# Kernel tuning notes

Measured on AMD Instinct MI355X. Metric: run time of the kernel, lower is better.

## Reference

```python
import jax, jax.numpy as jnp
import numpy as np

BN_EPS = 1e-5
NEG_SLOPE = 0.2


def _add_self_loops(edge_index, n):
    loops = jnp.arange(n, dtype=edge_index.dtype)
    src = jnp.concatenate([edge_index[0], loops])
    dst = jnp.concatenate([edge_index[1], loops])
    return src, dst


def _batchnorm(h, g, b):
    mean = h.mean(axis=0)
    var = h.var(axis=0)  # biased, as in BN forward
    return (h - mean) * jax.lax.rsqrt(var + BN_EPS) * g + b


def _gat_conv(x, edge_index, W, att_src, att_dst, bias):
    # heads=2, concat=False (mean over heads), add_self_loops=True
    n = x.shape[0]
    H, F = att_src.shape
    xp = (x @ W).reshape(n, H, F)                      # [N,H,F]
    a_src = jnp.einsum('nhf,hf->nh', xp, att_src)      # [N,H]
    a_dst = jnp.einsum('nhf,hf->nh', xp, att_dst)
    src, dst = _add_self_loops(edge_index, n)
    e = jax.nn.leaky_relu(a_src[src] + a_dst[dst], NEG_SLOPE)  # [Et,H]
    emax = jax.ops.segment_max(e, dst, num_segments=n)[dst]
    ex = jnp.exp(e - emax)
    denom = jax.ops.segment_sum(ex, dst, num_segments=n)[dst]
    alpha = ex / denom                                 # softmax per dst node
    msg = xp[src] * alpha[..., None]                   # [Et,H,F]
    out = jax.ops.segment_sum(msg, dst, num_segments=n)
    return out.mean(axis=1) + bias                     # [N,F]


def _gcn_conv(x, edge_index, W, bias):
    n = x.shape[0]
    xp = x @ W
    src, dst = _add_self_loops(edge_index, n)
    deg = jax.ops.segment_sum(jnp.ones_like(src, dtype=xp.dtype), dst, num_segments=n)
    dinv = jnp.where(deg > 0, jax.lax.rsqrt(jnp.maximum(deg, 1.0)), 0.0)
    norm = dinv[src] * dinv[dst]                       # [Et]
    out = jax.ops.segment_sum(xp[src] * norm[:, None], dst, num_segments=n)
    return out + bias


def setup_inputs() -> dict:
    key = jax.random.key(0)
    ks = jax.random.split(key, 16)
    N, E, D_IN, HID, LAT, DEC = 50000, 800000, 256, 128, 64, 256
    s = lambda fan: 1.0 / np.sqrt(fan)
    inp = {
        'x': jax.random.normal(ks[0], (N, D_IN), jnp.float32),
        'edge_index': jax.random.randint(ks[1], (2, E), 0, N, dtype=jnp.int32),
        'gat_W': jax.random.normal(ks[2], (D_IN, 2 * HID), jnp.float32) * s(D_IN),
        'gat_att_src': jax.random.normal(ks[3], (2, HID), jnp.float32) * s(HID),
        'gat_att_dst': jax.random.normal(ks[4], (2, HID), jnp.float32) * s(HID),
        'gat_bias': jnp.zeros((HID,), jnp.float32),
        'bn1_g': jnp.ones((HID,), jnp.float32),
        'bn1_b': jnp.zeros((HID,), jnp.float32),
        'gcn_W': jax.random.normal(ks[5], (HID, LAT), jnp.float32) * s(HID),
        'gcn_bias': jnp.zeros((LAT,), jnp.float32),
        'bn2_g': jnp.ones((LAT,), jnp.float32),
        'bn2_b': jnp.zeros((LAT,), jnp.float32),
        'mu_W': jax.random.normal(ks[6], (LAT, LAT), jnp.float32) * s(LAT),
        'mu_b': jnp.zeros((LAT,), jnp.float32),
        'lv_W': jax.random.normal(ks[7], (LAT, LAT), jnp.float32) * s(LAT),
        'lv_b': jnp.zeros((LAT,), jnp.float32),
        'res_W': jax.random.normal(ks[8], (LAT, LAT), jnp.float32) * s(LAT),
        'res_b': jnp.zeros((LAT,), jnp.float32),
        'dec_W1': jax.random.normal(ks[9], (2 * LAT, DEC), jnp.float32) * s(2 * LAT),
        'dec_b1': jnp.zeros((DEC,), jnp.float32),
        'dec_W2': jax.random.normal(ks[10], (DEC, 1), jnp.float32) * s(DEC),
        'dec_b2': jnp.zeros((1,), jnp.float32),
        'eps': jax.random.normal(ks[11], (N, LAT), jnp.float32),
    }
    return inp


def reference(x, edge_index, gat_W, gat_att_src, gat_att_dst, gat_bias,
              bn1_g, bn1_b, gcn_W, gcn_bias, bn2_g, bn2_b,
              mu_W, mu_b, lv_W, lv_b, res_W, res_b,
              dec_W1, dec_b1, dec_W2, dec_b2, eps):
    # encode (dropout omitted: eval mode; BN uses batch statistics)
    h = jax.nn.relu(_gat_conv(x, edge_index, gat_W, gat_att_src, gat_att_dst, gat_bias))
    h = _batchnorm(h, bn1_g, bn1_b)
    h = jax.nn.relu(_gcn_conv(h, edge_index, gcn_W, gcn_bias))
    h = _batchnorm(h, bn2_g, bn2_b)
    mu = h @ mu_W + mu_b
    logvar = h @ lv_W + lv_b
    # reparameterize
    z = mu + eps * jnp.exp(0.5 * logvar)
    # decode: edge-gather -> residual linear -> concat -> MLP
    res_z = z @ res_W + res_b
    row, col = edge_index[0], edge_index[1]
    e_emb = jnp.concatenate([res_z[row], res_z[col]], axis=1)  # [E, 2*LAT]
    hdec = jax.nn.relu(e_emb @ dec_W1 + dec_b1)
    recon = (hdec @ dec_W2 + dec_b2)[:, 0]
    return recon, mu, logvar
```

## Files before the change

### kernel.cpp

```cpp
#include <hip/hip_runtime.h>
#include <math.h>

constexpr int DIN = 256;
constexpr int HID = 128;
constexpr int LAT = 64;

typedef short bfrag __attribute__((ext_vector_type(8)));
typedef float f32x4 __attribute__((ext_vector_type(4)));

__device__ __forceinline__ float4 ld4(const float* p) { return *reinterpret_cast<const float4*>(p); }
__device__ __forceinline__ void st4(float* p, float4 v) { *reinterpret_cast<float4*>(p) = v; }

__device__ __forceinline__ unsigned short f2bf(float f) {
  unsigned int u = __float_as_uint(f);
  unsigned int r = (u + 0x7FFFu + ((u >> 16) & 1u)) >> 16;
  return (unsigned short)r;
}

__device__ __forceinline__ float bf2f(unsigned short u) {
  return __uint_as_float(((unsigned int)u) << 16);
}

__global__ __launch_bounds__(256) void gemm64b(const float* __restrict__ A, const float* __restrict__ B,
                                               const float* __restrict__ crow, unsigned short* __restrict__ Cb,
                                               int M, int N, int K) {
  __shared__ float As[32][68];
  __shared__ float Bs[32][68];
  int t = threadIdx.x;
  int m0 = blockIdx.x * 64, n0 = blockIdx.y * 64;
  int tm = t & 15, tn = t >> 4;
  float acc[4][4];
#pragma unroll
  for (int i = 0; i < 4; i++)
#pragma unroll
    for (int j = 0; j < 4; j++) acc[i][j] = 0.f;

  for (int kt = 0; kt < K; kt += 32) {
#pragma unroll
    for (int i = 0; i < 2; ++i) {
      int f4 = t + i * 256;
      int m = f4 >> 3;
      int k4 = (f4 & 7) << 2;
      int gm = m0 + m;
      float4 v = make_float4(0.f, 0.f, 0.f, 0.f);
      if (gm < M) v = ld4(A + (size_t)gm * K + kt + k4);
      As[k4 + 0][m] = v.x; As[k4 + 1][m] = v.y; As[k4 + 2][m] = v.z; As[k4 + 3][m] = v.w;
    }
#pragma unroll
    for (int i = 0; i < 2; ++i) {
      int f4 = t + i * 256;
      int k = f4 >> 4;
      int n4 = (f4 & 15) << 2;
      float4 v = ld4(B + (size_t)(kt + k) * N + n0 + n4);
      st4(&Bs[k][n4], v);
    }
    __syncthreads();
#pragma unroll
    for (int k = 0; k < 32; ++k) {
      float4 a = ld4(&As[k][tm << 2]);
      float4 b = ld4(&Bs[k][tn << 2]);
      float av[4] = {a.x, a.y, a.z, a.w};
      float bv[4] = {b.x, b.y, b.z, b.w};
#pragma unroll
      for (int i = 0; i < 4; i++)
#pragma unroll
        for (int j = 0; j < 4; j++) acc[i][j] = fmaf(av[i], bv[j], acc[i][j]);
    }
    __syncthreads();
  }
#pragma unroll
  for (int i = 0; i < 4; ++i) {
    int gm = m0 + (tm << 2) + i;
    if (gm < M) {
      int nb = n0 + (tn << 2);
      ushort4 o;
      o.x = f2bf(acc[i][0] + crow[nb]);
      o.y = f2bf(acc[i][1] + crow[nb + 1]);
      o.z = f2bf(acc[i][2] + crow[nb + 2]);
      o.w = f2bf(acc[i][3] + crow[nb + 3]);
      *(ushort4*)(Cb + (size_t)gm * N + nb) = o;
    }
  }
}

__global__ __launch_bounds__(256) void gemm_xp_mfma(const float* __restrict__ xf,
                                                    const unsigned short* __restrict__ Wtb,
                                                    const float* __restrict__ att_src,
                                                    const float* __restrict__ att_dst,
                                                    unsigned short* __restrict__ xpb,
                                                    float* __restrict__ a_src, float* __restrict__ a_dst, int M) {
  __shared__ unsigned short Als[64 * 256];
  __shared__ unsigned short Bls[64 * 256];
  int t = threadIdx.x;
  int wv = t >> 6, l = t & 63, lg = l >> 4, ll = l & 15;
  int cg = blockIdx.x;
  int rt = blockIdx.y;

  {
    int row = t >> 2, seg = t & 3;
    int gr = min(rt * 64 + row, M - 1);
    const float4* src = (const float4*)(xf + (size_t)gr * 256 + seg * 64);
    int swz = (row & 7) << 4;
#pragma unroll
    for (int c = 0; c < 8; ++c) {
      float4 a = src[2 * c], b = src[2 * c + 1];
      uint4 v;
      v.x = (unsigned)f2bf(a.x) | ((unsigned)f2bf(a.y) << 16);
      v.y = (unsigned)f2bf(a.z) | ((unsigned)f2bf(a.w) << 16);
      v.z = (unsigned)f2bf(b.x) | ((unsigned)f2bf(b.y) << 16);
      v.w = (unsigned)f2bf(b.z) | ((unsigned)f2bf(b.w) << 16);
      int bo = seg * 128 + c * 16;
      *(uint4*)((char*)Als + row * 512 + (bo ^ swz)) = v;
    }
  }
  {
    int col = t >> 2, seg = t & 3;
    const uint4* src = (const uint4*)(Wtb + (size_t)(cg * 64 + col) * 256 + seg * 64);
    int swz = (col & 7) << 4;
#pragma unroll
    for (int c = 0; c < 8; ++c) {
      int bo = seg * 128 + c * 16;
      *(uint4*)((char*)Bls + col * 512 + (bo ^ swz)) = src[c];
    }
  }
  __syncthreads();

  f32x4 acc[4];
#pragma unroll
  for (int i = 0; i < 4; ++i) acc[i] = (f32x4){0.f, 0.f, 0.f, 0.f};

#pragma unroll
  for (int kt = 0; kt < 8; ++kt) {
    int ar = wv * 16 + ll;
    bfrag af = *(const bfrag*)((char*)Als + ar * 512 + ((kt * 64 + lg * 16) ^ ((ar & 7) << 4)));
#pragma unroll
    for (int fn = 0; fn < 4; ++fn) {
      int bc = fn * 16 + ll;
      bfrag bf = *(const bfrag*)((char*)Bls + bc * 512 + ((kt * 64 + lg * 16) ^ ((bc & 7) << 4)));
      acc[fn] = __builtin_amdgcn_mfma_f32_16x16x32_bf16(af, bf, acc[fn], 0, 0, 0);
    }
  }

#pragma unroll
  for (int fn = 0; fn < 4; ++fn) {
#pragma unroll
    for (int r = 0; r < 4; ++r) {
      int row = rt * 64 + wv * 16 + lg * 4 + r;
      if (row < M) xpb[(size_t)row * 512 + cg * 64 + fn * 16 + ll] = f2bf(acc[fn][r]);
    }
  }

  int h = cg >> 1;
  int c0 = (cg & 1) * 64;
  float asv[4], adv[4];
#pragma unroll
  for (int fn = 0; fn < 4; ++fn) {
    asv[fn] = att_src[h * 128 + c0 + fn * 16 + ll];
    adv[fn] = att_dst[h * 128 + c0 + fn * 16 + ll];
  }
  float ps[4] = {0.f, 0.f, 0.f, 0.f}, pd[4] = {0.f, 0.f, 0.f, 0.f};
#pragma unroll
  for (int fn = 0; fn < 4; ++fn)
#pragma unroll
    for (int r = 0; r < 4; ++r) {
      ps[r] = fmaf(acc[fn][r], asv[fn], ps[r]);
      pd[r] = fmaf(acc[fn][r], adv[fn], pd[r]);
    }
#pragma unroll
  for (int m = 8; m >= 1; m >>= 1) {
#pragma unroll
    for (int r = 0; r < 4; ++r) { ps[r] += __shfl_xor(ps[r], m); pd[r] += __shfl_xor(pd[r], m); }
  }
  if (ll == 0) {
#pragma unroll
    for (int r = 0; r < 4; ++r) {
      int row = rt * 64 + wv * 16 + lg * 4 + r;
      if (row < M) {
        atomicAdd(&a_src[row * 2 + h], ps[r]);
        atomicAdd(&a_dst[row * 2 + h], pd[r]);
      }
    }
  }
}

__global__ void deg_count(const int* __restrict__ ei, int E, int Et, int* __restrict__ deg) {
  int i = blockIdx.x * blockDim.x + threadIdx.x;
  if (i >= Et) return;
  int d = (i < E) ? ei[E + i] : (i - E);
  atomicAdd(&deg[d], 1);
}

__global__ __launch_bounds__(256) void bsum_kernel(const int* __restrict__ deg, int N, int* __restrict__ bsum) {
  int t = threadIdx.x;
  int i = blockIdx.x * 256 + t;
  int v = (i < N) ? deg[i] : 0;
#pragma unroll
  for (int m = 32; m >= 1; m >>= 1) v += __shfl_xor(v, m);
  __shared__ int sh[4];
  if ((t & 63) == 0) sh[t >> 6] = v;
  __syncthreads();
  if (t == 0) bsum[blockIdx.x] = sh[0] + sh[1] + sh[2] + sh[3];
}

__global__ __launch_bounds__(256) void bscan_kernel(int* __restrict__ bsum, int B) {
  __shared__ int sh[256];
  int t = threadIdx.x;
  int v = (t < B) ? bsum[t] : 0;
  sh[t] = v;
  __syncthreads();
  for (int d = 1; d < 256; d <<= 1) {
    int x = (t >= d) ? sh[t - d] : 0;
    __syncthreads();
    sh[t] += x;
    __syncthreads();
  }
  if (t < B) bsum[t] = sh[t] - v;
}

__global__ __launch_bounds__(256) void scan_apply(const int* __restrict__ deg, const int* __restrict__ bsum, int N,
                                                  int* __restrict__ offs, int* __restrict__ cursor,
                                                  float* __restrict__ dinv) {
  int t = threadIdx.x;
  int i = blockIdx.x * 256 + t;
  int v = (i < N) ? deg[i] : 0;
  __shared__ int sh[256];
  sh[t] = v;
  __syncthreads();
  for (int d = 1; d < 256; d <<= 1) {
    int x = (t >= d) ? sh[t - d] : 0;
    __syncthreads();
    sh[t] += x;
    __syncthreads();
  }
  if (i < N) {
    int off = bsum[blockIdx.x] + sh[t] - v;
    offs[i] = off;
    cursor[i] = off;
    dinv[i] = rsqrtf((float)v);
  }
}

__global__ void csr_fill(const int* __restrict__ ei, int E, int Et, int* __restrict__ cursor, int* __restrict__ csr) {
  int i = blockIdx.x * blockDim.x + threadIdx.x;
  if (i >= Et) return;
  int s, d;
  if (i < E) { s = ei[i]; d = ei[E + i]; } else { s = i - E; d = i - E; }
  int pos = atomicAdd(&cursor[d], 1);
  csr[pos] = s;
}

__global__ __launch_bounds__(256) void gat_fused(const int* __restrict__ offs, const int* __restrict__ deg,
                                                 const int* __restrict__ csr, const float* __restrict__ a_src,
                                                 const float* __restrict__ a_dst,
                                                 const unsigned short* __restrict__ xpb,
                                                 const float* __restrict__ bias,
                                                 float* __restrict__ h1, int N) {
  int wid = threadIdx.x >> 6, lane = threadIdx.x & 63;
  int n = blockIdx.x * 4 + wid;
  if (n >= N) return;
  int off = offs[n], dg = deg[n];
  float ad0 = a_dst[n * 2], ad1 = a_dst[n * 2 + 1];
  const float2* as2 = (const float2*)a_src;

  float4 acc = make_float4(0.f, 0.f, 0.f, 0.f);
  float s0 = 0.f, s1 = 0.f;
  bool h0 = lane < 32;

#define GAT_STEP(aa, uu)                                         \
  {                                                              \
    float e0 = (aa).x + ad0; e0 = e0 >= 0.f ? e0 : 0.2f * e0;    \
    float e1 = (aa).y + ad1; e1 = e1 >= 0.f ? e1 : 0.2f * e1;    \
    float x0 = __expf(e0), x1 = __expf(e1);                      \
    s0 += x0; s1 += x1;                                          \
    float xa = h0 ? x0 : x1;                                     \
    acc.x = fmaf(bf2f((uu).x), xa, acc.x);                       \
    acc.y = fmaf(bf2f((uu).y), xa, acc.y);                       \
    acc.z = fmaf(bf2f((uu).z), xa, acc.z);                       \
    acc.w = fmaf(bf2f((uu).w), xa, acc.w);                       \
  }

  int k = 0;
  for (; k + 8 <= dg; k += 8) {
    int s_[8];
#pragma unroll
    for (int q = 0; q < 8; ++q) s_[q] = csr[off + k + q];
    float2 a_[8];
    ushort4 u_[8];
#pragma unroll
    for (int q = 0; q < 8; ++q) a_[q] = as2[s_[q]];
#pragma unroll
    for (int q = 0; q < 8; ++q) u_[q] = ((const ushort4*)(xpb + (size_t)s_[q] * 512))[lane];
#pragma unroll
    for (int q = 0; q < 8; ++q) GAT_STEP(a_[q], u_[q]);
  }
  for (; k + 4 <= dg; k += 4) {
    int sa = csr[off + k], sb = csr[off + k + 1], sc = csr[off + k + 2], sd = csr[off + k + 3];
    float2 aa = as2[sa], ab = as2[sb], ac = as2[sc], ad = as2[sd];
    ushort4 ua = ((const ushort4*)(xpb + (size_t)sa * 512))[lane];
    ushort4 ub = ((const ushort4*)(xpb + (size_t)sb * 512))[lane];
    ushort4 uc = ((const ushort4*)(xpb + (size_t)sc * 512))[lane];
    ushort4 ud = ((const ushort4*)(xpb + (size_t)sd * 512))[lane];
    GAT_STEP(aa, ua); GAT_STEP(ab, ub); GAT_STEP(ac, uc); GAT_STEP(ad, ud);
  }
  for (; k < dg; ++k) {
    int s = csr[off + k];
    float2 a = as2[s];
    ushort4 u = ((const ushort4*)(xpb + (size_t)s * 512))[lane];
    GAT_STEP(a, u);
  }
#undef GAT_STEP

  float r = h0 ? (1.f / s0) : (1.f / s1);
  acc.x *= r; acc.y *= r; acc.z *= r; acc.w *= r;

  float ox = __shfl_down(acc.x, 32);
  float oy = __shfl_down(acc.y, 32);
  float oz = __shfl_down(acc.z, 32);
  float ow = __shfl_down(acc.w, 32);
  if (h0) {
    int f4 = lane << 2;
    float4 b = ld4(bias + f4);
    float4 o;
    o.x = fmaxf(0.f, (acc.x + ox) * 0.5f + b.x);
    o.y = fmaxf(0.f, (acc.y + oy) * 0.5f + b.y);
    o.z = fmaxf(0.f, (acc.z + oz) * 0.5f + b.z);
    o.w = fmaxf(0.f, (acc.w + ow) * 0.5f + b.w);
    st4(h1 + (size_t)n * 128 + f4, o);
  }
}

template <int C>
__global__ __launch_bounds__(256) void bn_stats(const float* __restrict__ h, int N, float* __restrict__ P,
                                                float* __restrict__ PS) {
  constexpr int R = 256 / C;
  __shared__ float sh[256], sh2[256];
  int t = threadIdx.x;
  int c = t % C, r = t / C;
  float s = 0.f, ss = 0.f;
  for (int n = blockIdx.x * R + r; n < N; n += gridDim.x * R) {
    float v = h[(size_t)n * C + c];
    s += v; ss += v * v;
  }
  sh[t] = s; sh2[t] = ss;
  __syncthreads();
  if (r == 0) {
#pragma unroll
    for (int i = 1; i < R; ++i) { s += sh[i * C + c]; ss += sh2[i * C + c]; }
    P[blockIdx.x * C + c] = s;
    PS[blockIdx.x * C + c] = ss;
  }
}

__global__ __launch_bounds__(256) void bn_fold_gcn(const float* __restrict__ P, const float* __restrict__ PS,
                                                   int G, int N, const float* __restrict__ g,
                                                   const float* __restrict__ b, const float* __restrict__ W,
                                                   float* __restrict__ Wf, float* __restrict__ cvec) {
  __shared__ float ssv[128], stv[128];
  int t = threadIdx.x;
  if (t < 128) {
    float s = 0.f, ss = 0.f;
    for (int i = 0; i < G; ++i) { s += P[i * 128 + t]; ss += PS[i * 128 + t]; }
    float mean = s / N;
    float var = ss / N - mean * mean;
    float sc = g[t] * rsqrtf(var + 1e-5f);
    ssv[t] = sc;
    stv[t] = b[t] - mean * sc;
  }
  __syncthreads();
  for (int i = t; i < 128 * 64; i += 256) {
    int k = i >> 6;
    Wf[i] = ssv[k] * W[i];
  }
  if (t < 64) {
    float c = 0.f;
    for (int k = 0; k < 128; ++k) c += stv[k] * W[k * 64 + t];
    cvec[t] = c;
  }
}

__global__ __launch_bounds__(256) void bn_fold_mulv(const float* __restrict__ P, const float* __restrict__ PS,
                                                    int G, int N, const float* __restrict__ g,
                                                    const float* __restrict__ b,
                                                    const float* __restrict__ Wmu, const float* __restrict__ mub,
                                                    const float* __restrict__ Wlv, const float* __restrict__ lvb,
                                                    float* __restrict__ Wmuf, float* __restrict__ cmu,
                                                    float* __restrict__ Wlvf, float* __restrict__ clv) {
  __shared__ float ssv[64], stv[64];
  int t = threadIdx.x;
  if (t < 64) {
    float s = 0.f, ss = 0.f;
    for (int i = 0; i < G; ++i) { s += P[i * 64 + t]; ss += PS[i * 64 + t]; }
    float mean = s / N;
    float var = ss / N - mean * mean;
    float sc = g[t] * rsqrtf(var + 1e-5f);
    ssv[t] = sc;
    stv[t] = b[t] - mean * sc;
  }
  __syncthreads();
  for (int i = t; i < 4096; i += 256) {
    int k = i >> 6;
    Wmuf[i] = ssv[k] * Wmu[i];
    Wlvf[i] = ssv[k] * Wlv[i];
  }
  if (t < 64) {
    float cm = mub[t], cl = lvb[t];
    for (int k = 0; k < 64; ++k) { cm += stv[k] * Wmu[k * 64 + t]; cl += stv[k] * Wlv[k * 64 + t]; }
    cmu[t] = cm; clv[t] = cl;
  }
}

__global__ __launch_bounds__(256) void gcn_aggregate_bf(const int* __restrict__ offs, const int* __restrict__ deg,
                                                        const int* __restrict__ csr,
                                                        const unsigned short* __restrict__ xpb2,
                                                        const float* __restrict__ dinv, const float* __restrict__ bias,
                                                        float* __restrict__ g2, int N) {
  int wid = threadIdx.x >> 6, lane = threadIdx.x & 63;
  int n = blockIdx.x * 4 + wid;
  if (n >= N) return;
  int off = offs[n], dg = deg[n];
  float acc = 0.f;
  int k = 0;
  for (; k + 8 <= dg; k += 8) {
    int s_[8];
#pragma unroll
    for (int q = 0; q < 8; ++q) s_[q] = csr[off + k + q];
    float d_[8];
    unsigned short u_[8];
#pragma unroll
    for (int q = 0; q < 8; ++q) d_[q] = dinv[s_[q]];
#pragma unroll
    for (int q = 0; q < 8; ++q) u_[q] = xpb2[(size_t)s_[q] * 64 + lane];
#pragma unroll
    for (int q = 0; q < 8; ++q) acc = fmaf(bf2f(u_[q]), d_[q], acc);
  }
  for (; k + 4 <= dg; k += 4) {
    int sa = csr[off + k], sb = csr[off + k + 1], sc = csr[off + k + 2], sd = csr[off + k + 3];
    float da = dinv[sa], db = dinv[sb], dc = dinv[sc], dd = dinv[sd];
    unsigned short ua = xpb2[(size_t)sa * 64 + lane];
    unsigned short ub = xpb2[(size_t)sb * 64 + lane];
    unsigned short uc = xpb2[(size_t)sc * 64 + lane];
    unsigned short ud = xpb2[(size_t)sd * 64 + lane];
    acc = fmaf(bf2f(ua), da, acc);
    acc = fmaf(bf2f(ub), db, acc);
    acc = fmaf(bf2f(uc), dc, acc);
    acc = fmaf(bf2f(ud), dd, acc);
  }
  for (; k < dg; ++k) {
    int s = csr[off + k];
    acc = fmaf(bf2f(xpb2[(size_t)s * 64 + lane]), dinv[s], acc);
  }
  float v = acc * dinv[n] + bias[lane];
  g2[(size_t)n * 64 + lane] = fmaxf(v, 0.f);
}

__global__ __launch_bounds__(256) void tail_fused(const float* __restrict__ g2,
                                                  const float* __restrict__ Wmuf, const float* __restrict__ cmu,
                                                  const float* __restrict__ Wlvf, const float* __restrict__ clv,
                                                  const float* __restrict__ resW, const float* __restrict__ resb,
                                                  const float* __restrict__ eps,
                                                  float* __restrict__ mu, float* __restrict__ lv,
                                                  unsigned short* __restrict__ rzb, int N) {
  __shared__ float Gs[64][68];
  __shared__ float Wm[64][64];
  __shared__ float Wl[64][64];
  __shared__ float Rw[64][64];
  int t = threadIdx.x;
  int m0 = blockIdx.x * 64;
  int tm = t & 15, tn = t >> 4;

#pragma unroll
  for (int i = 0; i < 4; ++i) {
    int f4 = t + i * 256;
    int row = f4 >> 4;
    int k4 = (f4 & 15) << 2;
    int gr = m0 + row;
    float4 v = make_float4(0.f, 0.f, 0.f, 0.f);
    if (gr < N) v = ld4(g2 + (size_t)gr * 64 + k4);
    Gs[k4 + 0][row] = v.x; Gs[k4 + 1][row] = v.y; Gs[k4 + 2][row] = v.z; Gs[k4 + 3][row] = v.w;
    st4(&Wm[f4 >> 4][k4], ld4(Wmuf + f4 * 4));
    st4(&Wl[f4 >> 4][k4], ld4(Wlvf + f4 * 4));
    st4(&Rw[f4 >> 4][k4], ld4(resW + f4 * 4));
  }
  __syncthreads();

  float am[4][4], al[4][4];
#pragma unroll
  for (int i = 0; i < 4; ++i)
#pragma unroll
    for (int j = 0; j < 4; ++j) { am[i][j] = 0.f; al[i][j] = 0.f; }

#pragma unroll 8
  for (int k = 0; k < 64; ++k) {
    float4 a = ld4(&Gs[k][tm << 2]);
    float4 bm = ld4(&Wm[k][tn << 2]);
    float4 bl = ld4(&Wl[k][tn << 2]);
    float av[4] = {a.x, a.y, a.z, a.w};
    float bmv[4] = {bm.x, bm.y, bm.z, bm.w};
    float blv[4] = {bl.x, bl.y, bl.z, bl.w};
#pragma unroll
    for (int i = 0; i < 4; ++i)
#pragma unroll
      for (int j = 0; j < 4; ++j) {
        am[i][j] = fmaf(av[i], bmv[j], am[i][j]);
        al[i][j] = fmaf(av[i], blv[j], al[i][j]);
      }
  }

  int nb = tn << 2;
  float cm4[4] = {cmu[nb], cmu[nb + 1], cmu[nb + 2], cmu[nb + 3]};
  float cl4[4] = {clv[nb], clv[nb + 1], clv[nb + 2], clv[nb + 3]};
  float zreg[4][4];
#pragma unroll
  for (int i = 0; i < 4; ++i) {
    int gr = m0 + (tm << 2) + i;
    if (gr < N) {
      float4 ep = ld4(eps + (size_t)gr * 64 + nb);
      float epv[4] = {ep.x, ep.y, ep.z, ep.w};
      float muv[4], lvv[4];
#pragma unroll
      for (int j = 0; j < 4; ++j) {
        muv[j] = am[i][j] + cm4[j];
        lvv[j] = al[i][j] + cl4[j];
        zreg[i][j] = fmaf(epv[j], __expf(0.5f * lvv[j]), muv[j]);
      }
      st4(mu + (size_t)gr * 64 + nb, make_float4(muv[0], muv[1], muv[2], muv[3]));
      st4(lv + (size_t)gr * 64 + nb, make_float4(lvv[0], lvv[1], lvv[2], lvv[3]));
    } else {
#pragma unroll
      for (int j = 0; j < 4; ++j) zreg[i][j] = 0.f;
    }
  }

  __syncthreads();
#pragma unroll
  for (int i = 0; i < 4; ++i)
#pragma unroll
    for (int j = 0; j < 4; ++j) Gs[(tn << 2) + j][(tm << 2) + i] = zreg[i][j];
  __syncthreads();

  float ar[4][4];
#pragma unroll
  for (int i = 0; i < 4; ++i)
#pragma unroll
    for (int j = 0; j < 4; ++j) ar[i][j] = 0.f;
#pragma unroll 8
  for (int k = 0; k < 64; ++k) {
    float4 a = ld4(&Gs[k][tm << 2]);
    float4 b = ld4(&Rw[k][tn << 2]);
    float av[4] = {a.x, a.y, a.z, a.w};
    float bv[4] = {b.x, b.y, b.z, b.w};
#pragma unroll
    for (int i = 0; i < 4; ++i)
#pragma unroll
      for (int j = 0; j < 4; ++j) ar[i][j] = fmaf(av[i], bv[j], ar[i][j]);
  }
  float rb4[4] = {resb[nb], resb[nb + 1], resb[nb + 2], resb[nb + 3]};
#pragma unroll
  for (int i = 0; i < 4; ++i) {
    int gr = m0 + (tm << 2) + i;
    if (gr < N) {
      ushort4 o;
      o.x = f2bf(ar[i][0] + rb4[0]);
      o.y = f2bf(ar[i][1] + rb4[1]);
      o.z = f2bf(ar[i][2] + rb4[2]);
      o.w = f2bf(ar[i][3] + rb4[3]);
      *(ushort4*)(rzb + (size_t)gr * 64 + nb) = o;
    }
  }
}

__global__ void prep_gatW(const float* __restrict__ W, unsigned short* __restrict__ Wtb) {
  int i = blockIdx.x * blockDim.x + threadIdx.x;
  if (i >= 256 * 256) return;
  int col = i >> 8, k = i & 255;
  Wtb[i] = f2bf(W[k * 256 + col]);
}

__global__ void prep_W1(const float* __restrict__ W1, unsigned short* __restrict__ W1t) {
  int i = blockIdx.x * blockDim.x + threadIdx.x;
  if (i >= 4 * 256 * 40) return;
  int kt = i / 10240;
  int rem = i - kt * 10240;
  int j = rem / 40;
  int kp = rem - j * 40;
  float v = (kp < 32) ? W1[(size_t)(kt * 32 + kp) * 256 + j] : 0.f;
  W1t[i] = f2bf(v);
}

__global__ __launch_bounds__(256) void decoder_mfma(const int* __restrict__ ei, int E,
                                                    const unsigned short* __restrict__ rzb,
                                                    const unsigned short* __restrict__ W1t,
                                                    const float* __restrict__ b1, const float* __restrict__ W2,
                                                    const float* __restrict__ b2, float* __restrict__ recon) {
  __shared__ unsigned short Als[64 * 128];
  __shared__ unsigned short Bls[256 * 40];
  __shared__ float red[4][64];
  int t = threadIdx.x;
  int wv = t >> 6, l = t & 63;
  int lg = l >> 4, ll = l & 15;
  int e0 = blockIdx.x * 64;

  {
    int e = t >> 2;
    int part = (t >> 1) & 1;
    int half = t & 1;
    int eg = e0 + e;
    if (eg >= E) eg = E - 1;
    int r = (part == 0) ? ei[eg] : ei[E + eg];
    const uint4* gsrc = (const uint4*)(rzb + (size_t)r * 64 + half * 32);
    int bo0 = part * 128 + half * 64;
    int swz = (e & 7) << 4;
#pragma unroll
    for (int c = 0; c < 4; ++c) {
      uint4 v = gsrc[c];
      int bo = bo0 + c * 16;
      *(uint4*)&Als[e * 128 + ((bo ^ swz) >> 1)] = v;
    }
  }

  f32x4 acc[4][4];
#pragma unroll
  for (int a = 0; a < 4; ++a)
#pragma unroll
    for (int b = 0; b < 4; ++b) acc[a][b] = (f32x4){0.f, 0.f, 0.f, 0.f};

  for (int kt = 0; kt < 4; ++kt) {
    __syncthreads();
    {
      const uint4* gsrc = (const uint4*)(W1t + kt * 10240);
      uint4* ldst = (uint4*)Bls;
#pragma unroll
      for (int i = 0; i < 5; ++i) ldst[t + i * 256] = gsrc[t + i * 256];
    }
    __syncthreads();

    bfrag af[4];
#pragma unroll
    for (int fm = 0; fm < 4; ++fm) {
      int e = fm * 16 + ll;
      int bo = kt * 64 + lg * 16;
      af[fm] = *(const bfrag*)&Als[e * 128 + ((bo ^ ((e & 7) << 4)) >> 1)];
    }
#pragma unroll
    for (int fn = 0; fn < 4; ++fn) {
      int j = wv * 64 + fn * 16 + ll;
      bfrag bf = *(const bfrag*)&Bls[j * 40 + lg * 8];
#pragma unroll
      for (int fm = 0; fm < 4; ++fm)
        acc[fm][fn] = __builtin_amdgcn_mfma_f32_16x16x32_bf16(af[fm], bf, acc[fm][fn], 0, 0, 0);
    }
  }

  float bj[4], wj[4];
#pragma unroll
  for (int fn = 0; fn < 4; ++fn) {
    int j = wv * 64 + fn * 16 + ll;
    bj[fn] = b1[j];
    wj[fn] = W2[j];
  }
#pragma unroll
  for (int fm = 0; fm < 4; ++fm) {
    float pr[4] = {0.f, 0.f, 0.f, 0.f};
#pragma unroll
    for (int fn = 0; fn < 4; ++fn) {
#pragma unroll
      for (int r = 0; r < 4; ++r)
        pr[r] = fmaf(fmaxf(acc[fm][fn][r] + bj[fn], 0.f), wj[fn], pr[r]);
    }
#pragma unroll
    for (int m = 8; m >= 1; m >>= 1) {
#pragma unroll
      for (int r = 0; r < 4; ++r) pr[r] += __shfl_xor(pr[r], m);
    }
    if (ll == 0) {
#pragma unroll
      for (int r = 0; r < 4; ++r) red[wv][fm * 16 + lg * 4 + r] = pr[r];
    }
  }
  __syncthreads();
  if (t < 64) {
    int eg = e0 + t;
    if (eg < E) recon[eg] = red[0][t] + red[1][t] + red[2][t] + red[3][t] + b2[0];
  }
}

extern "C" void kernel_launch(void* const* d_in, const int* in_sizes, int n_in,
                              void* d_out, int out_size, void* d_ws, size_t ws_size,
                              hipStream_t stream) {
  const float* x = (const float*)d_in[0];
  const int* ei = (const int*)d_in[1];
  const float* gat_W = (const float*)d_in[2];
  const float* att_src = (const float*)d_in[3];
  const float* att_dst = (const float*)d_in[4];
  const float* gat_bias = (const float*)d_in[5];
  const float* bn1_g = (const float*)d_in[6];
  const float* bn1_b = (const float*)d_in[7];
  const float* gcn_W = (const float*)d_in[8];
  const float* gcn_bias = (const float*)d_in[9];
  const float* bn2_g = (const float*)d_in[10];
  const float* bn2_b = (const float*)d_in[11];
  const float* mu_W = (const float*)d_in[12];
  const float* mu_b = (const float*)d_in[13];
  const float* lv_W = (const float*)d_in[14];
  const float* lv_b = (const float*)d_in[15];
  const float* res_W = (const float*)d_in[16];
  const float* res_b = (const float*)d_in[17];
  const float* dec_W1 = (const float*)d_in[18];
  const float* dec_b1 = (const float*)d_in[19];
  const float* dec_W2 = (const float*)d_in[20];
  const float* dec_b2 = (const float*)d_in[21];
  const float* eps = (const float*)d_in[22];

  int N = in_sizes[0] / DIN;
  int E = in_sizes[1] / 2;
  int Et = E + N;
  int NB = (N + 255) / 256;

  float* ws = (float*)d_ws;
  size_t off = 0;
  float* xp = ws; off += (size_t)N * 256;
  unsigned short* xpb = (unsigned short*)xp;
  unsigned short* xpb2 = (unsigned short*)xp;
  float* g2 = xp + (size_t)N * 64;
  float* rz = xp + (size_t)N * 192;
  unsigned short* rzb = (unsigned short*)rz;
  float* h1 = ws + off; off += (size_t)N * 128;
  float* a_src = ws + off; off += (size_t)2 * N;
  float* a_dst = ws + off; off += (size_t)2 * N;
  float* dinv = ws + off; off += N;
  float* P = ws + off; off += 128 * 128;
  float* PS = ws + off; off += 128 * 128;
  float* W2f = ws + off; off += 128 * 64;
  float* c2 = ws + off; off += 64;
  float* Wmuf = ws + off; off += 64 * 64;
  float* cmu = ws + off; off += 64;
  float* Wlvf = ws + off; off += 64 * 64;
  float* clv = ws + off; off += 64;
  unsigned short* W1t = (unsigned short*)(ws + off); off += 20480;
  unsigned short* Wtb = (unsigned short*)(ws + off); off += 32768;
  int* deg = (int*)(ws + off); off += N;
  int* offs = (int*)(ws + off); off += N;
  int* cursor = (int*)(ws + off); off += N;
  int* bsum = (int*)(ws + off); off += 256;
  int* csr = (int*)(ws + off); off += Et;

  float* recon = (float*)d_out;
  float* mu = recon + E;
  float* lv = mu + (size_t)N * LAT;

  prep_W1<<<(4 * 256 * 40 + 255) / 256, 256, 0, stream>>>(dec_W1, W1t);
  prep_gatW<<<(256 * 256 + 255) / 256, 256, 0, stream>>>(gat_W, Wtb);
  hipMemsetAsync(a_src, 0, (size_t)4 * N * sizeof(float), stream);

  dim3 gX(4, (N + 63) / 64);
  gemm_xp_mfma<<<gX, 256, 0, stream>>>(x, Wtb, att_src, att_dst, xpb, a_src, a_dst, N);

  hipMemsetAsync(deg, 0, (size_t)N * sizeof(int), stream);
  deg_count<<<(Et + 255) / 256, 256, 0, stream>>>(ei, E, Et, deg);
  bsum_kernel<<<NB, 256, 0, stream>>>(deg, N, bsum);
  bscan_kernel<<<1, 256, 0, stream>>>(bsum, NB);
  scan_apply<<<NB, 256, 0, stream>>>(deg, bsum, N, offs, cursor, dinv);
  csr_fill<<<(Et + 255) / 256, 256, 0, stream>>>(ei, E, Et, cursor, csr);

  gat_fused<<<(N + 3) / 4, 256, 0, stream>>>(offs, deg, csr, a_src, a_dst, xpb, gat_bias, h1, N);

  bn_stats<128><<<128, 256, 0, stream>>>(h1, N, P, PS);
  bn_fold_gcn<<<1, 256, 0, stream>>>(P, PS, 128, N, bn1_g, bn1_b, gcn_W, W2f, c2);
  dim3 gB((N + 63) / 64, 1);
  gemm64b<<<gB, 256, 0, stream>>>(h1, W2f, c2, xpb2, N, 64, 128);

  gcn_aggregate_bf<<<(N + 3) / 4, 256, 0, stream>>>(offs, deg, csr, xpb2, dinv, gcn_bias, g2, N);

  bn_stats<64><<<128, 256, 0, stream>>>(g2, N, P, PS);
  bn_fold_mulv<<<1, 256, 0, stream>>>(P, PS, 128, N, bn2_g, bn2_b, mu_W, mu_b, lv_W, lv_b,
                                      Wmuf, cmu, Wlvf, clv);
  tail_fused<<<(N + 63) / 64, 256, 0, stream>>>(g2, Wmuf, cmu, Wlvf, clv, res_W, res_b, eps,
                                                mu, lv, rzb, N);

  decoder_mfma<<<(E + 63) / 64, 256, 0, stream>>>(ei, E, rzb, W1t, dec_b1, dec_W2, dec_b2, recon);
}
```

Before: 563.1 us.

## Use bf16 MFMA for GCN GEMM and split edge lists across half-waves

Replaces the scalar fp32 GEMM for the BN-folded GCN weight with a bf16 MFMA kernel. The folded weight is now stored transposed in bf16, and h1 is converted to bf16 in LDS. The GAT and GCN aggregation kernels now split each node's neighbor list between the two half-waves, each doing wider per-lane loads (uint4 / 32-bit), and combine partial sums and softmax denominators with shuffles. This aims to improve memory-level parallelism and cut per-edge instruction count. The cost is extra shuffles plus bf16 rounding of h1 and the weights inside the GEMM.

```diff
diff --git a/kernel.cpp b/kernel.cpp
--- a/kernel.cpp
+++ b/kernel.cpp
@@ -19,68 +19,6 @@
 
 __device__ __forceinline__ float bf2f(unsigned short u) {
   return __uint_as_float(((unsigned int)u) << 16);
-}
-
-__global__ __launch_bounds__(256) void gemm64b(const float* __restrict__ A, const float* __restrict__ B,
-                                               const float* __restrict__ crow, unsigned short* __restrict__ Cb,
-                                               int M, int N, int K) {
-  __shared__ float As[32][68];
-  __shared__ float Bs[32][68];
-  int t = threadIdx.x;
-  int m0 = blockIdx.x * 64, n0 = blockIdx.y * 64;
-  int tm = t & 15, tn = t >> 4;
-  float acc[4][4];
-#pragma unroll
-  for (int i = 0; i < 4; i++)
-#pragma unroll
-    for (int j = 0; j < 4; j++) acc[i][j] = 0.f;
-
-  for (int kt = 0; kt < K; kt += 32) {
-#pragma unroll
-    for (int i = 0; i < 2; ++i) {
-      int f4 = t + i * 256;
-      int m = f4 >> 3;
-      int k4 = (f4 & 7) << 2;
-      int gm = m0 + m;
-      float4 v = make_float4(0.f, 0.f, 0.f, 0.f);
-      if (gm < M) v = ld4(A + (size_t)gm * K + kt + k4);
-      As[k4 + 0][m] = v.x; As[k4 + 1][m] = v.y; As[k4 + 2][m] = v.z; As[k4 + 3][m] = v.w;
-    }
-#pragma unroll
-    for (int i = 0; i < 2; ++i) {
-      int f4 = t + i * 256;
-      int k = f4 >> 4;
-      int n4 = (f4 & 15) << 2;
-      float4 v = ld4(B + (size_t)(kt + k) * N + n0 + n4);
-      st4(&Bs[k][n4], v);
-    }
-    __syncthreads();
-#pragma unroll
-    for (int k = 0; k < 32; ++k) {
-      float4 a = ld4(&As[k][tm << 2]);
-      float4 b = ld4(&Bs[k][tn << 2]);
-      float av[4] = {a.x, a.y, a.z, a.w};
-      float bv[4] = {b.x, b.y, b.z, b.w};
-#pragma unroll
-      for (int i = 0; i < 4; i++)
-#pragma unroll
-        for (int j = 0; j < 4; j++) acc[i][j] = fmaf(av[i], bv[j], acc[i][j]);
-    }
-    __syncthreads();
-  }
-#pragma unroll
-  for (int i = 0; i < 4; ++i) {
-    int gm = m0 + (tm << 2) + i;
-    if (gm < M) {
-      int nb = n0 + (tn << 2);
-      ushort4 o;
-      o.x = f2bf(acc[i][0] + crow[nb]);
-      o.y = f2bf(acc[i][1] + crow[nb + 1]);
-      o.z = f2bf(acc[i][2] + crow[nb + 2]);
-      o.w = f2bf(acc[i][3] + crow[nb + 3]);
-      *(ushort4*)(Cb + (size_t)gm * N + nb) = o;
-    }
-  }
 }
 
 __global__ __launch_bounds__(256) void gemm_xp_mfma(const float* __restrict__ xf,
@@ -247,6 +185,21 @@
   if (i < E) { s = ei[i]; d = ei[E + i]; } else { s = i - E; d = i - E; }
   int pos = atomicAdd(&cursor[d], 1);
   csr[pos] = s;
+}
+
+__device__ __forceinline__ void gat_step(float2 aa, uint4 uu, float ad0, float ad1, bool headA,
+                                         float& s0, float& s1, float acc[8]) {
+  float e0 = aa.x + ad0; e0 = e0 >= 0.f ? e0 : 0.2f * e0;
+  float e1 = aa.y + ad1; e1 = e1 >= 0.f ? e1 : 0.2f * e1;
+  float x0 = __expf(e0), x1 = __expf(e1);
+  s0 += x0; s1 += x1;
+  float xa = headA ? x0 : x1;
+  unsigned v[4] = {uu.x, uu.y, uu.z, uu.w};
+#pragma unroll
+  for (int q = 0; q < 4; ++q) {
+    acc[2 * q]     = fmaf(bf2f((unsigned short)(v[q] & 0xFFFFu)), xa, acc[2 * q]);
+    acc[2 * q + 1] = fmaf(bf2f((unsigned short)(v[q] >> 16)), xa, acc[2 * q + 1]);
+  }
 }
 
 __global__ __launch_bounds__(256) void gat_fused(const int* __restrict__ offs, const int* __restrict__ deg,
@@ -261,71 +214,64 @@
   int off = offs[n], dg = deg[n];
   float ad0 = a_dst[n * 2], ad1 = a_dst[n * 2 + 1];
   const float2* as2 = (const float2*)a_src;
-
-  float4 acc = make_float4(0.f, 0.f, 0.f, 0.f);
+  int hl = lane & 31;
+  bool headA = hl < 16;
+  int dh = dg >> 1;
+  int st = (lane < 32) ? 0 : dh;
+  int en = (lane < 32) ? dh : dg;
+
+  float acc[8];
+#pragma unroll
+  for (int j = 0; j < 8; ++j) acc[j] = 0.f;
   float s0 = 0.f, s1 = 0.f;
-  bool h0 = lane < 32;
-
-#define GAT_STEP(aa, uu)                                         \
-  {                                                              \
-    float e0 = (aa).x + ad0; e0 = e0 >= 0.f ? e0 : 0.2f * e0;    \
-    float e1 = (aa).y + ad1; e1 = e1 >= 0.f ? e1 : 0.2f * e1;    \
-    float x0 = __expf(e0), x1 = __expf(e1);                      \
-    s0 += x0; s1 += x1;                                          \
-    float xa = h0 ? x0 : x1;                                     \
-    acc.x = fmaf(bf2f((uu).x), xa, acc.x);                       \
-    acc.y = fmaf(bf2f((uu).y), xa, acc.y);                       \
-    acc.z = fmaf(bf2f((uu).z), xa, acc.z);                       \
-    acc.w = fmaf(bf2f((uu).w), xa, acc.w);                       \
-  }
-
-  int k = 0;
-  for (; k + 8 <= dg; k += 8) {
+
+  int k = st;
+  for (; k + 8 <= en; k += 8) {
     int s_[8];
+    float2 a_[8];
+    uint4 u_[8];
 #pragma unroll
     for (int q = 0; q < 8; ++q) s_[q] = csr[off + k + q];
-    float2 a_[8];
-    ushort4 u_[8];
 #pragma unroll
     for (int q = 0; q < 8; ++q) a_[q] = as2[s_[q]];
 #pragma unroll
-    for (int q = 0; q < 8; ++q) u_[q] = ((const ushort4*)(xpb + (size_t)s_[q] * 512))[lane];
-#pragma unroll
-    for (int q = 0; q < 8; ++q) GAT_STEP(a_[q], u_[q]);
-  }
-  for (; k + 4 <= dg; k += 4) {
-    int sa = csr[off + k], sb = csr[off + k + 1], sc = csr[off + k + 2], sd = csr[off + k + 3];
-    float2 aa = as2[sa], ab = as2[sb], ac = as2[sc], ad = as2[sd];
-    ushort4 ua = ((const ushort4*)(xpb + (size_t)sa * 512))[lane];
-    ushort4 ub = ((const ushort4*)(xpb + (size_t)sb * 512))[lane];
-    ushort4 uc = ((const ushort4*)(xpb + (size_t)sc * 512))[lane];
-    ushort4 ud = ((const ushort4*)(xpb + (size_t)sd * 512))[lane];
-    GAT_STEP(aa, ua); GAT_STEP(ab, ub); GAT_STEP(ac, uc); GAT_STEP(ad, ud);
-  }
-  for (; k < dg; ++k) {
+    for (int q = 0; q < 8; ++q) u_[q] = *(const uint4*)(xpb + (size_t)s_[q] * 512 + 8 * hl);
+#pragma unroll
+    for (int q = 0; q < 8; ++q) gat_step(a_[q], u_[q], ad0, ad1, headA, s0, s1, acc);
+  }
+  for (; k < en; ++k) {
     int s = csr[off + k];
     float2 a = as2[s];
-    ushort4 u = ((const ushort4*)(xpb + (size_t)s * 512))[lane];
-    GAT_STEP(a, u);
-  }
-#undef GAT_STEP
-
-  float r = h0 ? (1.f / s0) : (1.f / s1);
-  acc.x *= r; acc.y *= r; acc.z *= r; acc.w *= r;
-
-  float ox = __shfl_down(acc.x, 32);
-  float oy = __shfl_down(acc.y, 32);
-  float oz = __shfl_down(acc.z, 32);
-  float ow = __shfl_down(acc.w, 32);
-  if (h0) {
-    int f4 = lane << 2;
-    float4 b = ld4(bias + f4);
-    float4 o;
-    o.x = fmaxf(0.f, (acc.x + ox) * 0.5f + b.x);
-    o.y = fmaxf(0.f, (acc.y + oy) * 0.5f + b.y);
-    o.z = fmaxf(0.f, (acc.z + oz) * 0.5f + b.z);
-    o.w = fmaxf(0.f, (acc.w + ow) * 0.5f + b.w);
-    st4(h1 + (size_t)n * 128 + f4, o);
+    uint4 u = *(const uint4*)(xpb + (size_t)s * 512 + 8 * hl);
+    gat_step(a, u, ad0, ad1, headA, s0, s1, acc);
+  }
+
+#pragma unroll
+  for (int j = 0; j < 8; ++j) acc[j] += __shfl_down(acc[j], 32);
+  s0 += __shfl_down(s0, 32);
+  s1 += __shfl_down(s1, 32);
+
+  if (lane < 32) {
+    float r = headA ? (1.f / s0) : (1.f / s1);
+#pragma unroll
+    for (int j = 0; j < 8; ++j) acc[j] *= r;
+    float oth[8];
+#pragma unroll
+    for (int j = 0; j < 8; ++j) oth[j] = __shfl_down(acc[j], 16);
+    if (headA) {
+      int f0 = 8 * hl;
+      float4 b0 = ld4(bias + f0);
+      float4 b1 = ld4(bias + f0 + 4);
+      float o[8];
+#pragma unroll
+      for (int j = 0; j < 8; ++j) o[j] = (acc[j] + oth[j]) * 0.5f;
+      float4 w0 = make_float4(fmaxf(o[0] + b0.x, 0.f), fmaxf(o[1] + b0.y, 0.f),
+                              fmaxf(o[2] + b0.z, 0.f), fmaxf(o[3] + b0.w, 0.f));
+      float4 w1 = make_float4(fmaxf(o[4] + b1.x, 0.f), fmaxf(o[5] + b1.y, 0.f),
+                              fmaxf(o[6] + b1.z, 0.f), fmaxf(o[7] + b1.w, 0.f));
+      st4(h1 + (size_t)n * 128 + f0, w0);
+      st4(h1 + (size_t)n * 128 + f0 + 4, w1);
+    }
   }
 }
 
@@ -354,7 +300,7 @@
 __global__ __launch_bounds__(256) void bn_fold_gcn(const float* __restrict__ P, const float* __restrict__ PS,
                                                    int G, int N, const float* __restrict__ g,
                                                    const float* __restrict__ b, const float* __restrict__ W,
-                                                   float* __restrict__ Wf, float* __restrict__ cvec) {
+                                                   unsigned short* __restrict__ Wtb2, float* __restrict__ cvec) {
   __shared__ float ssv[128], stv[128];
   int t = threadIdx.x;
   if (t < 128) {
@@ -367,9 +313,9 @@
     stv[t] = b[t] - mean * sc;
   }
   __syncthreads();
-  for (int i = t; i < 128 * 64; i += 256) {
-    int k = i >> 6;
-    Wf[i] = ssv[k] * W[i];
+  for (int i = t; i < 64 * 128; i += 256) {
+    int j = i >> 7, k = i & 127;
+    Wtb2[i] = f2bf(ssv[k] * W[k * 64 + j]);
   }
   if (t < 64) {
     float c = 0.f;
@@ -406,6 +352,72 @@
     float cm = mub[t], cl = lvb[t];
     for (int k = 0; k < 64; ++k) { cm += stv[k] * Wmu[k * 64 + t]; cl += stv[k] * Wlv[k * 64 + t]; }
     cmu[t] = cm; clv[t] = cl;
+  }
+}
+
+__global__ __launch_bounds__(256) void gemm_h1_mfma(const float* __restrict__ h1,
+                                                    const unsigned short* __restrict__ Wtb2,
+                                                    const float* __restrict__ cvec,
+                                                    unsigned short* __restrict__ xpb2, int M) {
+  __shared__ unsigned short Als[64 * 128];
+  __shared__ unsigned short Bls[64 * 128];
+  int t = threadIdx.x;
+  int wv = t >> 6, l = t & 63, lg = l >> 4, ll = l & 15;
+  int m0 = blockIdx.x * 64;
+
+  {
+    int row = t >> 2, seg = t & 3;
+    int gr = min(m0 + row, M - 1);
+    const float4* src = (const float4*)(h1 + (size_t)gr * 128 + seg * 32);
+    int swz = (row & 7) << 4;
+#pragma unroll
+    for (int c = 0; c < 4; ++c) {
+      float4 a = src[2 * c], b = src[2 * c + 1];
+      uint4 v;
+      v.x = (unsigned)f2bf(a.x) | ((unsigned)f2bf(a.y) << 16);
+      v.y = (unsigned)f2bf(a.z) | ((unsigned)f2bf(a.w) << 16);
+      v.z = (unsigned)f2bf(b.x) | ((unsigned)f2bf(b.y) << 16);
+      v.w = (unsigned)f2bf(b.z) | ((unsigned)f2bf(b.w) << 16);
+      int bo = seg * 64 + c * 16;
+      *(uint4*)((char*)Als + row * 256 + (bo ^ swz)) = v;
+    }
+  }
+  {
+    int col = t >> 2, seg = t & 3;
+    const uint4* src = (const uint4*)(Wtb2 + col * 128 + seg * 32);
+    int swz = (col & 7) << 4;
+#pragma unroll
+    for (int c = 0; c < 4; ++c) {
+      int bo = seg * 64 + c * 16;
+      *(uint4*)((char*)Bls + col * 256 + (bo ^ swz)) = src[c];
+    }
+  }
+  __syncthreads();
+
+  f32x4 acc[4];
+#pragma unroll
+  for (int i = 0; i < 4; ++i) acc[i] = (f32x4){0.f, 0.f, 0.f, 0.f};
+
+#pragma unroll
+  for (int kt = 0; kt < 4; ++kt) {
+    int ar = wv * 16 + ll;
+    bfrag af = *(const bfrag*)((char*)Als + ar * 256 + ((kt * 64 + lg * 16) ^ ((ar & 7) << 4)));
+#pragma unroll
+    for (int fn = 0; fn < 4; ++fn) {
+      int bc = fn * 16 + ll;
+      bfrag bf = *(const bfrag*)((char*)Bls + bc * 256 + ((kt * 64 + lg * 16) ^ ((bc & 7) << 4)));
+      acc[fn] = __builtin_amdgcn_mfma_f32_16x16x32_bf16(af, bf, acc[fn], 0, 0, 0);
+    }
+  }
+
+#pragma unroll
+  for (int fn = 0; fn < 4; ++fn) {
+    float cv = cvec[fn * 16 + ll];
+#pragma unroll
+    for (int r = 0; r < 4; ++r) {
+      int row = m0 + wv * 16 + lg * 4 + r;
+      if (row < M) xpb2[(size_t)row * 64 + fn * 16 + ll] = f2bf(acc[fn][r] + cv);
+    }
   }
 }
 
@@ -418,39 +430,45 @@
   int n = blockIdx.x * 4 + wid;
   if (n >= N) return;
   int off = offs[n], dg = deg[n];
-  float acc = 0.f;
-  int k = 0;
-  for (; k + 8 <= dg; k += 8) {
+  int hl = lane & 31;
+  int dh = dg >> 1;
+  int st = (lane < 32) ? 0 : dh;
+  int en = (lane < 32) ? dh : dg;
+  float ax = 0.f, ay = 0.f;
+  int k = st;
+  for (; k + 8 <= en; k += 8) {
     int s_[8];
+    float d_[8];
+    unsigned u_[8];
 #pragma unroll
     for (int q = 0; q < 8; ++q) s_[q] = csr[off + k + q];
-    float d_[8];
-    unsigned short u_[8];
 #pragma unroll
     for (int q = 0; q < 8; ++q) d_[q] = dinv[s_[q]];
 #pragma unroll
-    for (int q = 0; q < 8; ++q) u_[q] = xpb2[(size_t)s_[q] * 64 + lane];
-#pragma unroll
-    for (int q = 0; q < 8; ++q) acc = fmaf(bf2f(u_[q]), d_[q], acc);
-  }
-  for (; k + 4 <= dg; k += 4) {
-    int sa = csr[off + k], sb = csr[off + k + 1], sc = csr[off + k + 2], sd = csr[off + k + 3];
-    float da = dinv[sa], db = dinv[sb], dc = dinv[sc], dd = dinv[sd];
-    unsigned short ua = xpb2[(size_t)sa * 64 + lane];
-    unsigned short ub = xpb2[(size_t)sb * 64 + lane];
-    unsigned short uc = xpb2[(size_t)sc * 64 + lane];
-    unsigned short ud = xpb2[(size_t)sd * 64 + lane];
-    acc = fmaf(bf2f(ua), da, acc);
-    acc = fmaf(bf2f(ub), db, acc);
-    acc = fmaf(bf2f(uc), dc, acc);
-    acc = fmaf(bf2f(ud), dd, acc);
-  }
-  for (; k < dg; ++k) {
+    for (int q = 0; q < 8; ++q) u_[q] = *(const unsigned*)(xpb2 + (size_t)s_[q] * 64 + 2 * hl);
+#pragma unroll
+    for (int q = 0; q < 8; ++q) {
+      ax = fmaf(bf2f((unsigned short)(u_[q] & 0xFFFFu)), d_[q], ax);
+      ay = fmaf(bf2f((unsigned short)(u_[q] >> 16)), d_[q], ay);
+    }
+  }
+  for (; k < en; ++k) {
     int s = csr[off + k];
-    acc = fmaf(bf2f(xpb2[(size_t)s * 64 + lane]), dinv[s], acc);
-  }
-  float v = acc * dinv[n] + bias[lane];
-  g2[(size_t)n * 64 + lane] = fmaxf(v, 0.f);
+    float d = dinv[s];
+    unsigned u = *(const unsigned*)(xpb2 + (size_t)s * 64 + 2 * hl);
+    ax = fmaf(bf2f((unsigned short)(u & 0xFFFFu)), d, ax);
+    ay = fmaf(bf2f((unsigned short)(u >> 16)), d, ay);
+  }
+  ax += __shfl_down(ax, 32);
+  ay += __shfl_down(ay, 32);
+  if (lane < 32) {
+    float dn = dinv[n];
+    float2 b = *(const float2*)(bias + 2 * hl);
+    float2 o;
+    o.x = fmaxf(ax * dn + b.x, 0.f);
+    o.y = fmaxf(ay * dn + b.y, 0.f);
+    *(float2*)(g2 + (size_t)n * 64 + 2 * hl) = o;
+  }
 }
 
 __global__ __launch_bounds__(256) void tail_fused(const float* __restrict__ g2,
@@ -730,7 +748,7 @@
   float* dinv = ws + off; off += N;
   float* P = ws + off; off += 128 * 128;
   float* PS = ws + off; off += 128 * 128;
-  float* W2f = ws + off; off += 128 * 64;
+  unsigned short* Wtb2 = (unsigned short*)(ws + off); off += 128 * 64;
   float* c2 = ws + off; off += 64;
   float* Wmuf = ws + off; off += 64 * 64;
   float* cmu = ws + off; off += 64;
@@ -765,9 +783,8 @@
   gat_fused<<<(N + 3) / 4, 256, 0, stream>>>(offs, deg, csr, a_src, a_dst, xpb, gat_bias, h1, N);
 
   bn_stats<128><<<128, 256, 0, stream>>>(h1, N, P, PS);
-  bn_fold_gcn<<<1, 256, 0, stream>>>(P, PS, 128, N, bn1_g, bn1_b, gcn_W, W2f, c2);
-  dim3 gB((N + 63) / 64, 1);
-  gemm64b<<<gB, 256, 0, stream>>>(h1, W2f, c2, xpb2, N, 64, 128);
+  bn_fold_gcn<<<1, 256, 0, stream>>>(P, PS, 128, N, bn1_g, bn1_b, gcn_W, Wtb2, c2);
+  gemm_h1_mfma<<<(N + 63) / 64, 256, 0, stream>>>(h1, Wtb2, c2, xpb2, N);
 
   gcn_aggregate_bf<<<(N + 3) / 4, 256, 0, stream>>>(offs, deg, csr, xpb2, dinv, gcn_bias, g2, N);
 
```

Result: slower. 575.0 us (+2.1%).
